# Kernel tuning notes

Hardware: AMD Instinct MI355X
Metric: run time of the kernel (lower is better)

## Reference

```python
import jax, jax.numpy as jnp
import numpy as np

B, T, D, H = 2, 2048, 1024, 16
HD = D // H  # head_dim = 64


def setup_inputs() -> dict:
    key = jax.random.key(0)
    ks = jax.random.split(key, 6)
    x = jax.random.normal(ks[0], (B, T, D), dtype=jnp.float32)
    wq = jax.random.normal(ks[1], (D, D), dtype=jnp.float32) * (D ** -0.5)
    wk = jax.random.normal(ks[2], (D, D), dtype=jnp.float32) * (D ** -0.5)
    wv = jax.random.normal(ks[3], (D, D), dtype=jnp.float32) * (D ** -0.5)
    wo = jax.random.normal(ks[4], (D, D), dtype=jnp.float32) * (D ** -0.5)
    # RoPE tables: standard inverse-frequency angles, shape [T, head_dim]
    inv_freq = 1.0 / (10000.0 ** (jnp.arange(0, HD, 2, dtype=jnp.float32) / HD))
    ang = jnp.arange(T, dtype=jnp.float32)[:, None] * inv_freq[None, :]  # [T, HD/2]
    ang = jnp.concatenate([ang, ang], axis=-1)  # [T, HD]
    cos, sin = jnp.cos(ang), jnp.sin(ang)
    # causal mask [1,1,T,T]: True where attention is allowed
    mask = jnp.tril(jnp.ones((T, T), dtype=bool))[None, None]
    return {"x": x, "wq": wq, "wk": wk, "wv": wv, "wo": wo,
            "cos": cos, "sin": sin, "mask": mask}


def rotate_half(u):
    u1, u2 = jnp.split(u, 2, axis=-1)
    return jnp.concatenate([-u2, u1], axis=-1)


def reference(x, wq, wk, wv, wo, cos, sin, mask):
    b, t, c = x.shape
    # projections (nn.Linear: y = x @ W^T), reshape to [B, H, T, HD]
    def proj(w):
        return (x @ w.T).reshape(b, t, H, HD).transpose(0, 2, 1, 3)
    q, k, v = proj(wq), proj(wk), proj(wv)
    # inline RoPE: cos/sin broadcast [1,1,T,HD]
    co = cos[:t][None, None]
    si = sin[:t][None, None]
    q = q * co + rotate_half(q) * si
    k = k * co + rotate_half(k) * si
    # scaled dot-product attention with causal mask
    att = jnp.einsum("bhqd,bhkd->bhqk", q, k) * (HD ** -0.5)
    att = jnp.where(mask[:, :, :t, :t], att, -jnp.inf)
    att = jax.nn.softmax(att, axis=-1)
    out = jnp.einsum("bhqk,bhkd->bhqd", att, v)
    out = out.transpose(0, 2, 1, 3).reshape(b, t, c)
    return out @ wo.T
```

## Files before the change

kernel.cpp:

```cpp
#include <hip/hip_runtime.h>
#include <hip/hip_bf16.h>
#include <type_traits>

#define B_  2
#define T_  2048
#define D_  1024
#define H_  16
#define HD_ 64

typedef __attribute__((ext_vector_type(8))) short bf16x8;
typedef __attribute__((ext_vector_type(4))) float f32x4;

__device__ __forceinline__ unsigned short f2b(float x) {
  union { __hip_bfloat16 h; unsigned short u; } c;
  c.h = __float2bfloat16(x);
  return c.u;
}
__device__ __forceinline__ float b2f(unsigned short u) {
  union { unsigned short u; __hip_bfloat16 h; } c;
  c.u = u;
  return __bfloat162float(c.h);
}

__device__ __forceinline__ void ld_g2l_16(const unsigned short* g, unsigned short* l) {
  auto gp = (const __attribute__((address_space(1))) unsigned int*)g;
  auto lp = (__attribute__((address_space(3))) unsigned int*)l;
  __builtin_amdgcn_global_load_lds(gp, lp, 16, 0, 0);
}

__global__ void __launch_bounds__(256)
cast_all(const float* __restrict__ x, const float* __restrict__ wq,
         const float* __restrict__ wk, const float* __restrict__ wv,
         const float* __restrict__ wo, unsigned short* __restrict__ xb,
         unsigned short* __restrict__ wp) {
  int blk = blockIdx.x;
  const float* src;
  unsigned short* dst;
  size_t off;
  if (blk < 2048) {
    src = x; dst = xb; off = (size_t)blk * 2048;
  } else {
    int t = (blk - 2048) >> 9;
    int r = (blk - 2048) & 511;
    src = (t == 0) ? wq : (t == 1) ? wk : (t == 2) ? wv : wo;
    dst = wp + (size_t)t * 1048576;
    off = (size_t)r * 2048;
  }
  size_t i = off + threadIdx.x * 8;
  float4 a = *(const float4*)(src + i);
  float4 b = *(const float4*)(src + i + 4);
  unsigned short h[8] = {f2b(a.x), f2b(a.y), f2b(a.z), f2b(a.w),
                         f2b(b.x), f2b(b.y), f2b(b.z), f2b(b.w)};
  *(uint4*)(dst + i) = *(uint4*)h;
}

template <typename OutT, int MROWS>
__device__ __forceinline__ void gemm_core(const unsigned short* __restrict__ A,
                                          const unsigned short* __restrict__ Bw,
                                          OutT* __restrict__ C, int K, int Ldc,
                                          int rope_mode, const float* __restrict__ cosT,
                                          const float* __restrict__ sinT, int tok0) {
  constexpr int MT = MROWS / 32;
  __shared__ unsigned short a_s[2][MROWS * 32];
  __shared__ unsigned short b_s[2][128 * 32];
  const int tid = threadIdx.x;
  const int lane = tid & 63;
  const int w = tid >> 6;
  const int m16 = lane & 15;
  const int quad = lane >> 4;
  const int wm = w >> 1, wn = w & 1;
  const int rl = lane >> 2;
  const int cl = (lane & 3) * 8;

  f32x4 acc[MT][4];
#pragma unroll
  for (int i = 0; i < MT; i++)
#pragma unroll
    for (int j = 0; j < 4; j++) acc[i][j] = (f32x4){0.f, 0.f, 0.f, 0.f};

  auto stage = [&](int it, int bs) {
    int k0 = it * 32;
#pragma unroll
    for (int t = 0; t < MROWS / 64; t++) {
      int seg = w * 16 + t * 64;
      ld_g2l_16(A + (size_t)(seg + rl) * K + k0 + cl, &a_s[bs][seg * 32]);
    }
#pragma unroll
    for (int j2 = 0; j2 < 2; j2++) {
      int seg = w * 32 + j2 * 16;
      ld_g2l_16(Bw + (size_t)(seg + rl) * K + k0 + cl, &b_s[bs][seg * 32]);
    }
  };

  const int nit = K / 32;
  stage(0, 0);
  __syncthreads();
  for (int it = 0; it < nit; it++) {
    int cur = it & 1;
    if (it + 1 < nit) stage(it + 1, cur ^ 1);
    bf16x8 af[MT], bfr[4];
#pragma unroll
    for (int mt = 0; mt < MT; mt++)
      af[mt] = *(const bf16x8*)&a_s[cur][(wm * (MT * 16) + mt * 16 + m16) * 32 + quad * 8];
#pragma unroll
    for (int nt = 0; nt < 4; nt++)
      bfr[nt] = *(const bf16x8*)&b_s[cur][(wn * 64 + nt * 16 + m16) * 32 + quad * 8];
#pragma unroll
    for (int mt = 0; mt < MT; mt++)
#pragma unroll
      for (int nt = 0; nt < 4; nt++)
        acc[mt][nt] = __builtin_amdgcn_mfma_f32_16x16x32_bf16(af[mt], bfr[nt], acc[mt][nt], 0, 0, 0);
    __syncthreads();
  }

  if (rope_mode) {
    float scale = (rope_mode == 2) ? 0.18033688011112042f : 1.f;
#pragma unroll
    for (int mt = 0; mt < MT; mt++)
#pragma unroll
      for (int reg = 0; reg < 4; reg++) {
        int t = (tok0 + wm * (MT * 16) + mt * 16 + quad * 4 + reg) & (T_ - 1);
#pragma unroll
        for (int nt = 0; nt < 2; nt++) {
          int d = nt * 16 + m16;
          float co = cosT[t * HD_ + d] * scale;
          float si = sinT[t * HD_ + d] * scale;
          float lo = acc[mt][nt][reg], hi = acc[mt][nt + 2][reg];
          acc[mt][nt][reg]     = lo * co - hi * si;
          acc[mt][nt + 2][reg] = hi * co + lo * si;
        }
      }
  }
#pragma unroll
  for (int mt = 0; mt < MT; mt++)
#pragma unroll
    for (int nt = 0; nt < 4; nt++)
#pragma unroll
      for (int reg = 0; reg < 4; reg++) {
        OutT* p = C + (size_t)(wm * (MT * 16) + mt * 16 + quad * 4 + reg) * Ldc + wn * 64 + nt * 16 + m16;
        if constexpr (std::is_same_v<OutT, float>) *p = acc[mt][nt][reg];
        else *p = f2b(acc[mt][nt][reg]);
      }
}

__global__ void __launch_bounds__(256)
gemm_qkv(const unsigned short* __restrict__ xb, const unsigned short* __restrict__ wp,
         unsigned short* __restrict__ qkv, const float* __restrict__ cosT,
         const float* __restrict__ sinT) {
  const int nb = blockIdx.x;
  const int bm = blockIdx.y * 128;
  const int mi = nb >> 3;
  const int bn = (nb & 7) * 128;
  const int rope_mode = (mi == 0) ? 2 : (mi == 1) ? 1 : 0;
  gemm_core<unsigned short, 128>(xb + (size_t)bm * D_,
                                 wp + (size_t)(mi * 1024 + bn) * D_,
                                 qkv + (size_t)mi * (4096ull * D_) + (size_t)bm * D_ + bn,
                                 D_, D_, rope_mode, cosT, sinT, bm);
}

__global__ void __launch_bounds__(256)
gemm_out(const unsigned short* __restrict__ Ab, const unsigned short* __restrict__ wob,
         float* __restrict__ C) {
  const int bn = blockIdx.x * 128;
  const int bm = blockIdx.y * 64;
  gemm_core<float, 64>(Ab + (size_t)bm * D_, wob + (size_t)bn * D_,
                       C + (size_t)bm * D_ + bn, D_, D_, 0, nullptr, nullptr, 0);
}

__global__ void __launch_bounds__(256)
vtrans(const unsigned short* __restrict__ V, unsigned short* __restrict__ VT) {
  __shared__ unsigned short tile[64][72];
  const int tid = threadIdx.x;
  const int tb = blockIdx.x, h = blockIdx.y, b = blockIdx.z;
  const unsigned short* Vb = V + ((size_t)b * T_ + tb * 64) * D_ + h * HD_;
  int r = tid >> 2;
  int c = (tid & 3) * 16;
  bf16x8 v0 = *(const bf16x8*)(Vb + (size_t)r * D_ + c);
  bf16x8 v1 = *(const bf16x8*)(Vb + (size_t)r * D_ + c + 8);
#pragma unroll
  for (int e = 0; e < 8; e++) tile[c + e][r] = ((unsigned short*)&v0)[e];
#pragma unroll
  for (int e = 0; e < 8; e++) tile[c + 8 + e][r] = ((unsigned short*)&v1)[e];
  __syncthreads();
  unsigned short* VTb = VT + ((size_t)b * H_ + h) * HD_ * T_ + tb * 64;
  *(bf16x8*)(VTb + (size_t)r * T_ + c)     = *(const bf16x8*)&tile[r][c];
  *(bf16x8*)(VTb + (size_t)r * T_ + c + 8) = *(const bf16x8*)&tile[r][c + 8];
}

__global__ void __launch_bounds__(512, 4)
attn_kernel(const unsigned short* __restrict__ Q, const unsigned short* __restrict__ K,
            const unsigned short* __restrict__ VT, unsigned short* __restrict__ O) {
  __shared__ __align__(16) unsigned short qp_s[128][72];
  __shared__ __align__(16) unsigned short k_s[2][64 * 64];
  __shared__ __align__(16) unsigned short vt_s[2][64 * 64];

  const int tid = threadIdx.x;
  const int lane = tid & 63;
  const int w = tid >> 6;
  const int m16 = lane & 15;
  const int quad = lane >> 4;
  const int swz = m16 & 7;
  const int pc0 = quad ^ swz;
  const int pc1 = pc0 ^ 4;

  int x = blockIdx.x;
  int bh, qb;
  if (x < 256) { bh = x >> 4; qb = x & 15; }
  else         { bh = 16 + ((x - 256) >> 4); qb = 15 - ((x - 256) & 15); }
  const int b = bh >> 4, h = bh & 15;
  const int q0 = qb * 128;

  const unsigned short* Qb = Q + ((size_t)b * T_ + q0) * D_ + h * HD_;
  const unsigned short* Kb = K + (size_t)b * T_ * D_ + h * HD_;
  const unsigned short* VTb = VT + ((size_t)b * H_ + h) * HD_ * T_;

#pragma unroll
  for (int i = 0; i < 2; i++) {
    int idx = tid + i * 512;
    int r = idx >> 3, c = idx & 7;
    *(bf16x8*)&qp_s[r][c * 8] = *(const bf16x8*)(Qb + (size_t)r * D_ + c * 8);
  }

  auto stage_kv = [&](int kt, int bs) {
    int r_sub = lane >> 3, c = lane & 7;
    int cs = (c ^ r_sub) * 8;
    int gr = w * 8 + r_sub;
    ld_g2l_16(Kb + (size_t)(kt * 64 + gr) * D_ + cs, &k_s[bs][w * 8 * 64]);
    ld_g2l_16(VTb + (size_t)gr * T_ + kt * 64 + cs, &vt_s[bs][w * 8 * 64]);
  };

  f32x4 o_acc[4];
#pragma unroll
  for (int dt = 0; dt < 4; dt++) o_acc[dt] = (f32x4){0.f, 0.f, 0.f, 0.f};
  float m_i = -1e30f, l_i = 0.f;
  const int rg = q0 + w * 16 + m16;
  const int rmax = q0 + w * 16 + 15;
  const int ktmax = (q0 + 127) >> 6;

  stage_kv(0, 0);
  __syncthreads();
  bf16x8 q_frag[2];
  q_frag[0] = *(const bf16x8*)&qp_s[w * 16 + m16][quad * 8];
  q_frag[1] = *(const bf16x8*)&qp_s[w * 16 + m16][32 + quad * 8];

  for (int kt = 0; kt <= ktmax; kt++) {
    int cur = kt & 1;
    if (kt < ktmax) stage_kv(kt + 1, cur ^ 1);

    if (kt * 64 <= rmax) {
      const unsigned short* kc = &k_s[cur][0];
      const unsigned short* vc = &vt_s[cur][0];
      f32x4 sf[4];
      __builtin_amdgcn_s_setprio(1);
#pragma unroll
      for (int jt = 0; jt < 4; jt++) {
        bf16x8 a0 = *(const bf16x8*)&kc[(jt * 16 + m16) * 64 + pc0 * 8];
        bf16x8 a1 = *(const bf16x8*)&kc[(jt * 16 + m16) * 64 + pc1 * 8];
        f32x4 acc = (f32x4){0.f, 0.f, 0.f, 0.f};
        acc = __builtin_amdgcn_mfma_f32_16x16x32_bf16(a0, q_frag[0], acc, 0, 0, 0);
        acc = __builtin_amdgcn_mfma_f32_16x16x32_bf16(a1, q_frag[1], acc, 0, 0, 0);
        sf[jt] = acc;
      }
      __builtin_amdgcn_s_setprio(0);
      if (kt * 64 + 63 > q0 + w * 16) {
#pragma unroll
        for (int jt = 0; jt < 4; jt++)
#pragma unroll
          for (int reg = 0; reg < 4; reg++) {
            int jg = kt * 64 + jt * 16 + quad * 4 + reg;
            if (jg > rg) sf[jt][reg] = -1e30f;
          }
      }
      float mx = sf[0][0];
#pragma unroll
      for (int jt = 0; jt < 4; jt++)
#pragma unroll
        for (int reg = 0; reg < 4; reg++) mx = fmaxf(mx, sf[jt][reg]);
      mx = fmaxf(mx, __shfl_xor(mx, 16, 64));
      mx = fmaxf(mx, __shfl_xor(mx, 32, 64));
      if (__all(mx <= m_i + 8.f)) {
      } else {
        float mn = fmaxf(m_i, mx);
        float alpha = exp2f(m_i - mn);
        l_i *= alpha;
#pragma unroll
        for (int dt = 0; dt < 4; dt++)
#pragma unroll
          for (int reg = 0; reg < 4; reg++) o_acc[dt][reg] *= alpha;
        m_i = mn;
      }
      float lt = 0.f;
      float p[4][4];
#pragma unroll
      for (int jt = 0; jt < 4; jt++)
#pragma unroll
        for (int reg = 0; reg < 4; reg++) {
          p[jt][reg] = exp2f(sf[jt][reg] - m_i);
          lt += p[jt][reg];
        }
      lt += __shfl_xor(lt, 16, 64);
      lt += __shfl_xor(lt, 32, 64);
      l_i += lt;
#pragma unroll
      for (int jt = 0; jt < 4; jt++) {
        unsigned short pk[4] = {f2b(p[jt][0]), f2b(p[jt][1]), f2b(p[jt][2]), f2b(p[jt][3])};
        *(uint2*)&qp_s[w * 16 + m16][jt * 16 + quad * 4] = *(uint2*)pk;
      }
      bf16x8 bp0 = *(const bf16x8*)&qp_s[w * 16 + m16][quad * 8];
      bf16x8 bp1 = *(const bf16x8*)&qp_s[w * 16 + m16][32 + quad * 8];
      __builtin_amdgcn_s_setprio(1);
#pragma unroll
      for (int dt = 0; dt < 4; dt++) {
        int rowd = dt * 16 + m16;
        bf16x8 a0 = *(const bf16x8*)&vc[rowd * 64 + pc0 * 8];
        bf16x8 a1 = *(const bf16x8*)&vc[rowd * 64 + pc1 * 8];
        o_acc[dt] = __builtin_amdgcn_mfma_f32_16x16x32_bf16(a0, bp0, o_acc[dt], 0, 0, 0);
        o_acc[dt] = __builtin_amdgcn_mfma_f32_16x16x32_bf16(a1, bp1, o_acc[dt], 0, 0, 0);
      }
      __builtin_amdgcn_s_setprio(0);
    }
    __syncthreads();
  }

  float inv = 1.f / l_i;
#pragma unroll
  for (int dt = 0; dt < 4; dt++) {
    unsigned short ok[4];
#pragma unroll
    for (int reg = 0; reg < 4; reg++) ok[reg] = f2b(o_acc[dt][reg] * inv);
    *(uint2*)&qp_s[w * 16 + m16][dt * 16 + quad * 4] = *(uint2*)ok;
  }
  __syncthreads();
  unsigned short* Ob = O + ((size_t)b * T_ + q0) * D_ + h * HD_;
#pragma unroll
  for (int i = 0; i < 2; i++) {
    int idx = tid + i * 512;
    int r = idx >> 3, c = idx & 7;
    *(bf16x8*)(Ob + (size_t)r * D_ + c * 8) = *(const bf16x8*)&qp_s[r][c * 8];
  }
}

extern "C" void kernel_launch(void* const* d_in, const int* in_sizes, int n_in,
                              void* d_out, int out_size, void* d_ws, size_t ws_size,
                              hipStream_t stream) {
  const float* x    = (const float*)d_in[0];
  const float* wq   = (const float*)d_in[1];
  const float* wk   = (const float*)d_in[2];
  const float* wv   = (const float*)d_in[3];
  const float* wo   = (const float*)d_in[4];
  const float* cosT = (const float*)d_in[5];
  const float* sinT = (const float*)d_in[6];
  float* out = (float*)d_out;

  const size_t NTOK = (size_t)B_ * T_;
  const size_t SZ   = NTOK * D_;
  unsigned short* xb   = (unsigned short*)d_ws;
  unsigned short* Wp   = xb + SZ;
  unsigned short* QKVh = Wp + 4 * 1048576;
  unsigned short* Ab   = QKVh + 3 * SZ;
  unsigned short* VTb  = xb;

  cast_all<<<4096, 256, 0, stream>>>(x, wq, wk, wv, wo, xb, Wp);
  gemm_qkv<<<dim3(24, 32), 256, 0, stream>>>(xb, Wp, QKVh, cosT, sinT);
  vtrans<<<dim3(32, 16, 2), 256, 0, stream>>>(QKVh + 2 * SZ, VTb);
  attn_kernel<<<512, 512, 0, stream>>>(QKVh, QKVh + SZ, VTb, Ab);
  gemm_out<<<dim3(8, 64), 256, 0, stream>>>(Ab, Wp + 3 * 1048576, out);
}
```

Before: 219.7 us.

## Shrink attention query tile to 64 rows with 256-thread blocks

The attention kernel now handles 64 query rows per block with 4 waves instead of 128 rows with 8 waves, launching 1024 blocks. Blocks are ordered longest-first (query tile 31 down to 0) to balance the causal workload, and the per-wave skip test for fully masked key tiles is dropped because every wave now needs every staged tile. The row-sum shuffle reduction is moved after the PV MFMAs so it can overlap with them. In exchange, each K/V tile fetched from global memory is reused by half as many query rows, and each thread now issues four async loads per stage instead of two.

```diff
diff --git a/kernel.cpp b/kernel.cpp
--- a/kernel.cpp
+++ b/kernel.cpp
@@ -187,10 +187,10 @@
   *(bf16x8*)(VTb + (size_t)r * T_ + c + 8) = *(const bf16x8*)&tile[r][c + 8];
 }
 
-__global__ void __launch_bounds__(512, 4)
+__global__ void __launch_bounds__(256, 3)
 attn_kernel(const unsigned short* __restrict__ Q, const unsigned short* __restrict__ K,
             const unsigned short* __restrict__ VT, unsigned short* __restrict__ O) {
-  __shared__ __align__(16) unsigned short qp_s[128][72];
+  __shared__ __align__(16) unsigned short qp_s[64][72];
   __shared__ __align__(16) unsigned short k_s[2][64 * 64];
   __shared__ __align__(16) unsigned short vt_s[2][64 * 64];
 
@@ -203,12 +203,11 @@
   const int pc0 = quad ^ swz;
   const int pc1 = pc0 ^ 4;
 
-  int x = blockIdx.x;
-  int bh, qb;
-  if (x < 256) { bh = x >> 4; qb = x & 15; }
-  else         { bh = 16 + ((x - 256) >> 4); qb = 15 - ((x - 256) & 15); }
+  const int x = blockIdx.x;
+  const int qt = 31 - (x >> 5);
+  const int bh = x & 31;
   const int b = bh >> 4, h = bh & 15;
-  const int q0 = qb * 128;
+  const int q0 = qt * 64;
 
   const unsigned short* Qb = Q + ((size_t)b * T_ + q0) * D_ + h * HD_;
   const unsigned short* Kb = K + (size_t)b * T_ * D_ + h * HD_;
@@ -216,17 +215,19 @@
 
 #pragma unroll
   for (int i = 0; i < 2; i++) {
-    int idx = tid + i * 512;
+    int idx = tid + i * 256;
     int r = idx >> 3, c = idx & 7;
     *(bf16x8*)&qp_s[r][c * 8] = *(const bf16x8*)(Qb + (size_t)r * D_ + c * 8);
   }
 
   auto stage_kv = [&](int kt, int bs) {
-    int r_sub = lane >> 3, c = lane & 7;
-    int cs = (c ^ r_sub) * 8;
-    int gr = w * 8 + r_sub;
-    ld_g2l_16(Kb + (size_t)(kt * 64 + gr) * D_ + cs, &k_s[bs][w * 8 * 64]);
-    ld_g2l_16(VTb + (size_t)gr * T_ + kt * 64 + cs, &vt_s[bs][w * 8 * 64]);
+    int rs = lane >> 3;
+    int cs = ((lane & 7) ^ rs) * 8;
+    int gr = w * 16 + rs;
+    ld_g2l_16(Kb + (size_t)(kt * 64 + gr) * D_ + cs,      &k_s[bs][(w * 16) * 64]);
+    ld_g2l_16(Kb + (size_t)(kt * 64 + gr + 8) * D_ + cs,  &k_s[bs][(w * 16 + 8) * 64]);
+    ld_g2l_16(VTb + (size_t)gr * T_ + kt * 64 + cs,       &vt_s[bs][(w * 16) * 64]);
+    ld_g2l_16(VTb + (size_t)(gr + 8) * T_ + kt * 64 + cs, &vt_s[bs][(w * 16 + 8) * 64]);
   };
 
   f32x4 o_acc[4];
@@ -234,8 +235,6 @@
   for (int dt = 0; dt < 4; dt++) o_acc[dt] = (f32x4){0.f, 0.f, 0.f, 0.f};
   float m_i = -1e30f, l_i = 0.f;
   const int rg = q0 + w * 16 + m16;
-  const int rmax = q0 + w * 16 + 15;
-  const int ktmax = (q0 + 127) >> 6;
 
   stage_kv(0, 0);
   __syncthreads();
@@ -243,82 +242,79 @@
   q_frag[0] = *(const bf16x8*)&qp_s[w * 16 + m16][quad * 8];
   q_frag[1] = *(const bf16x8*)&qp_s[w * 16 + m16][32 + quad * 8];
 
-  for (int kt = 0; kt <= ktmax; kt++) {
-    int cur = kt & 1;
-    if (kt < ktmax) stage_kv(kt + 1, cur ^ 1);
-
-    if (kt * 64 <= rmax) {
-      const unsigned short* kc = &k_s[cur][0];
-      const unsigned short* vc = &vt_s[cur][0];
-      f32x4 sf[4];
-      __builtin_amdgcn_s_setprio(1);
-#pragma unroll
-      for (int jt = 0; jt < 4; jt++) {
-        bf16x8 a0 = *(const bf16x8*)&kc[(jt * 16 + m16) * 64 + pc0 * 8];
-        bf16x8 a1 = *(const bf16x8*)&kc[(jt * 16 + m16) * 64 + pc1 * 8];
-        f32x4 acc = (f32x4){0.f, 0.f, 0.f, 0.f};
-        acc = __builtin_amdgcn_mfma_f32_16x16x32_bf16(a0, q_frag[0], acc, 0, 0, 0);
-        acc = __builtin_amdgcn_mfma_f32_16x16x32_bf16(a1, q_frag[1], acc, 0, 0, 0);
-        sf[jt] = acc;
+  for (int t = 0; t <= qt; t++) {
+    int cur = t & 1;
+    if (t < qt) stage_kv(t + 1, cur ^ 1);
+
+    const unsigned short* kc = &k_s[cur][0];
+    const unsigned short* vc = &vt_s[cur][0];
+    f32x4 sf[4];
+    __builtin_amdgcn_s_setprio(1);
+#pragma unroll
+    for (int jt = 0; jt < 4; jt++) {
+      bf16x8 a0 = *(const bf16x8*)&kc[(jt * 16 + m16) * 64 + pc0 * 8];
+      bf16x8 a1 = *(const bf16x8*)&kc[(jt * 16 + m16) * 64 + pc1 * 8];
+      f32x4 acc = (f32x4){0.f, 0.f, 0.f, 0.f};
+      acc = __builtin_amdgcn_mfma_f32_16x16x32_bf16(a0, q_frag[0], acc, 0, 0, 0);
+      acc = __builtin_amdgcn_mfma_f32_16x16x32_bf16(a1, q_frag[1], acc, 0, 0, 0);
+      sf[jt] = acc;
+    }
+    __builtin_amdgcn_s_setprio(0);
+    if (t == qt) {
+#pragma unroll
+      for (int jt = 0; jt < 4; jt++)
+#pragma unroll
+        for (int reg = 0; reg < 4; reg++) {
+          int jg = t * 64 + jt * 16 + quad * 4 + reg;
+          if (jg > rg) sf[jt][reg] = -1e30f;
+        }
+    }
+    float mx = sf[0][0];
+#pragma unroll
+    for (int jt = 0; jt < 4; jt++)
+#pragma unroll
+      for (int reg = 0; reg < 4; reg++) mx = fmaxf(mx, sf[jt][reg]);
+    mx = fmaxf(mx, __shfl_xor(mx, 16, 64));
+    mx = fmaxf(mx, __shfl_xor(mx, 32, 64));
+    if (!__all(mx <= m_i + 8.f)) {
+      float mn = fmaxf(m_i, mx);
+      float alpha = exp2f(m_i - mn);
+      l_i *= alpha;
+#pragma unroll
+      for (int dt = 0; dt < 4; dt++)
+#pragma unroll
+        for (int reg = 0; reg < 4; reg++) o_acc[dt][reg] *= alpha;
+      m_i = mn;
+    }
+    float lt = 0.f;
+    float p[4][4];
+#pragma unroll
+    for (int jt = 0; jt < 4; jt++)
+#pragma unroll
+      for (int reg = 0; reg < 4; reg++) {
+        p[jt][reg] = exp2f(sf[jt][reg] - m_i);
+        lt += p[jt][reg];
       }
-      __builtin_amdgcn_s_setprio(0);
-      if (kt * 64 + 63 > q0 + w * 16) {
-#pragma unroll
-        for (int jt = 0; jt < 4; jt++)
-#pragma unroll
-          for (int reg = 0; reg < 4; reg++) {
-            int jg = kt * 64 + jt * 16 + quad * 4 + reg;
-            if (jg > rg) sf[jt][reg] = -1e30f;
-          }
-      }
-      float mx = sf[0][0];
-#pragma unroll
-      for (int jt = 0; jt < 4; jt++)
-#pragma unroll
-        for (int reg = 0; reg < 4; reg++) mx = fmaxf(mx, sf[jt][reg]);
-      mx = fmaxf(mx, __shfl_xor(mx, 16, 64));
-      mx = fmaxf(mx, __shfl_xor(mx, 32, 64));
-      if (__all(mx <= m_i + 8.f)) {
-      } else {
-        float mn = fmaxf(m_i, mx);
-        float alpha = exp2f(m_i - mn);
-        l_i *= alpha;
-#pragma unroll
-        for (int dt = 0; dt < 4; dt++)
-#pragma unroll
-          for (int reg = 0; reg < 4; reg++) o_acc[dt][reg] *= alpha;
-        m_i = mn;
-      }
-      float lt = 0.f;
-      float p[4][4];
-#pragma unroll
-      for (int jt = 0; jt < 4; jt++)
-#pragma unroll
-        for (int reg = 0; reg < 4; reg++) {
-          p[jt][reg] = exp2f(sf[jt][reg] - m_i);
-          lt += p[jt][reg];
-        }
-      lt += __shfl_xor(lt, 16, 64);
-      lt += __shfl_xor(lt, 32, 64);
-      l_i += lt;
-#pragma unroll
-      for (int jt = 0; jt < 4; jt++) {
-        unsigned short pk[4] = {f2b(p[jt][0]), f2b(p[jt][1]), f2b(p[jt][2]), f2b(p[jt][3])};
-        *(uint2*)&qp_s[w * 16 + m16][jt * 16 + quad * 4] = *(uint2*)pk;
-      }
-      bf16x8 bp0 = *(const bf16x8*)&qp_s[w * 16 + m16][quad * 8];
-      bf16x8 bp1 = *(const bf16x8*)&qp_s[w * 16 + m16][32 + quad * 8];
-      __builtin_amdgcn_s_setprio(1);
-#pragma unroll
-      for (int dt = 0; dt < 4; dt++) {
-        int rowd = dt * 16 + m16;
-        bf16x8 a0 = *(const bf16x8*)&vc[rowd * 64 + pc0 * 8];
-        bf16x8 a1 = *(const bf16x8*)&vc[rowd * 64 + pc1 * 8];
-        o_acc[dt] = __builtin_amdgcn_mfma_f32_16x16x32_bf16(a0, bp0, o_acc[dt], 0, 0, 0);
-        o_acc[dt] = __builtin_amdgcn_mfma_f32_16x16x32_bf16(a1, bp1, o_acc[dt], 0, 0, 0);
-      }
-      __builtin_amdgcn_s_setprio(0);
-    }
+#pragma unroll
+    for (int jt = 0; jt < 4; jt++) {
+      unsigned short pk[4] = {f2b(p[jt][0]), f2b(p[jt][1]), f2b(p[jt][2]), f2b(p[jt][3])};
+      *(uint2*)&qp_s[w * 16 + m16][jt * 16 + quad * 4] = *(uint2*)pk;
+    }
+    bf16x8 bp0 = *(const bf16x8*)&qp_s[w * 16 + m16][quad * 8];
+    bf16x8 bp1 = *(const bf16x8*)&qp_s[w * 16 + m16][32 + quad * 8];
+    __builtin_amdgcn_s_setprio(1);
+#pragma unroll
+    for (int dt = 0; dt < 4; dt++) {
+      int rowd = dt * 16 + m16;
+      bf16x8 a0 = *(const bf16x8*)&vc[rowd * 64 + pc0 * 8];
+      bf16x8 a1 = *(const bf16x8*)&vc[rowd * 64 + pc1 * 8];
+      o_acc[dt] = __builtin_amdgcn_mfma_f32_16x16x32_bf16(a0, bp0, o_acc[dt], 0, 0, 0);
+      o_acc[dt] = __builtin_amdgcn_mfma_f32_16x16x32_bf16(a1, bp1, o_acc[dt], 0, 0, 0);
+    }
+    __builtin_amdgcn_s_setprio(0);
+    lt += __shfl_xor(lt, 16, 64);
+    lt += __shfl_xor(lt, 32, 64);
+    l_i += lt;
     __syncthreads();
   }
 
@@ -334,7 +330,7 @@
   unsigned short* Ob = O + ((size_t)b * T_ + q0) * D_ + h * HD_;
 #pragma unroll
   for (int i = 0; i < 2; i++) {
-    int idx = tid + i * 512;
+    int idx = tid + i * 256;
     int r = idx >> 3, c = idx & 7;
     *(bf16x8*)(Ob + (size_t)r * D_ + c * 8) = *(const bf16x8*)&qp_s[r][c * 8];
   }
@@ -363,6 +359,6 @@
   cast_all<<<4096, 256, 0, stream>>>(x, wq, wk, wv, wo, xb, Wp);
   gemm_qkv<<<dim3(24, 32), 256, 0, stream>>>(xb, Wp, QKVh, cosT, sinT);
   vtrans<<<dim3(32, 16, 2), 256, 0, stream>>>(QKVh + 2 * SZ, VTb);
-  attn_kernel<<<512, 512, 0, stream>>>(QKVh, QKVh + SZ, VTb, Ab);
+  attn_kernel<<<1024, 256, 0, stream>>>(QKVh, QKVh + SZ, VTb, Ab);
   gemm_out<<<dim3(8, 64), 256, 0, stream>>>(Ab, Wp + 3 * 1048576, out);
 }
```

Measured after the change: 203.2 us. 1.08x faster.
